# Kernel optimization log

Hardware: AMD Instinct MI355X
Metric: run time of the kernel (lower is better)

The kernel has to match this reference:

```python
import jax, jax.numpy as jnp
import numpy as np

N = 100000      # nodes
E = 1600000     # edges (avg degree 16)
F_IN = 64
HID = 128
OUT = 64


def setup_inputs() -> dict:
    key = jax.random.key(0)
    ks = jax.random.split(key, 12)
    s = lambda k, i, o: jax.random.normal(k, (i, o), jnp.float32) / np.sqrt(i)
    x = jax.random.normal(ks[0], (N, F_IN), jnp.float32)
    edge_index = jax.random.randint(ks[1], (2, E), 0, N, dtype=jnp.int64)
    return {
        "x": x,
        "edge_index": edge_index,
        # conv1: SAGEConv(F_IN -> HID): lin_l (neighbors, with bias), lin_r (root)
        "W1n": s(ks[2], F_IN, HID), "b1n": jnp.zeros((HID,), jnp.float32),
        "W1r": s(ks[3], F_IN, HID),
        # lin1: Linear(F_IN -> HID)
        "Wl1": s(ks[4], F_IN, HID), "bl1": jnp.zeros((HID,), jnp.float32),
        # conv2: SAGEConv(HID -> OUT)
        "W2n": s(ks[5], HID, OUT), "b2n": jnp.zeros((OUT,), jnp.float32),
        "W2r": s(ks[6], HID, OUT),
        # lin2: Linear(HID -> OUT)
        "Wl2": s(ks[7], HID, OUT), "bl2": jnp.zeros((OUT,), jnp.float32),
    }


def _sage(x, src, dst, Wn, bn, Wr):
    # mean aggregation of source-node features at destination nodes
    msg = x[src]                                             # [E, F]
    agg = jax.ops.segment_sum(msg, dst, num_segments=N)      # [N, F]
    deg = jax.ops.segment_sum(jnp.ones((src.shape[0],), x.dtype), dst,
                              num_segments=N)                # [N]
    mean = agg / jnp.maximum(deg, 1.0)[:, None]
    return mean @ Wn + bn + x @ Wr


def reference(x, edge_index, W1n, b1n, W1r, Wl1, bl1, W2n, b2n, W2r, Wl2, bl2):
    src, dst = edge_index[0], edge_index[1]
    h = _sage(x, src, dst, W1n, b1n, W1r) + (x @ Wl1 + bl1)
    h = jax.nn.relu(h)
    out = _sage(h, src, dst, W2n, b2n, W2r) + (h @ Wl2 + bl2)
    return out
```

## Files before the change

### kernel.cpp

```cpp
#include <hip/hip_runtime.h>


#define NN 100000
#define NE 1600000
#define NSB 98
#define CAP2 18432
#define EPB 6250

typedef __attribute__((ext_vector_type(8))) __bf16 bf16x8;
typedef __attribute__((ext_vector_type(4))) float f32x4;

__device__ __forceinline__ float b2f(unsigned short u) {
    unsigned v = ((unsigned)u) << 16;
    float f;
    __builtin_memcpy(&f, &v, 4);
    return f;
}
__device__ __forceinline__ float b2f_lo(unsigned v) {
    unsigned w = v << 16;
    float f;
    __builtin_memcpy(&f, &w, 4);
    return f;
}
__device__ __forceinline__ float b2f_hi(unsigned v) {
    unsigned w = v & 0xFFFF0000u;
    float f;
    __builtin_memcpy(&f, &w, 4);
    return f;
}
__device__ __forceinline__ unsigned short f2b(float f) {
    unsigned u;
    __builtin_memcpy(&u, &f, 4);
    u += 0x7FFFu + ((u >> 16) & 1u);
    return (unsigned short)(u >> 16);
}

__global__ void sniff_kernel(const int* __restrict__ ei,
                             const unsigned int* __restrict__ xw,
                             int* __restrict__ flags, int* __restrict__ cntP) {
    __shared__ int s_or[256];
    __shared__ int s_cnt[256];
    int tid = threadIdx.x;
    if (tid < NSB) cntP[tid * 16] = 0;
    s_or[tid] = ei[2 * tid + 1];
    unsigned e = (xw[tid] >> 7) & 0xFFu;
    s_cnt[tid] = (e > 0x85u) ? 1 : 0;
    __syncthreads();
    for (int s = 128; s > 0; s >>= 1) {
        if (tid < s) { s_or[tid] |= s_or[tid + s]; s_cnt[tid] += s_cnt[tid + s]; }
        __syncthreads();
    }
    if (tid == 0) {
        flags[0] = (s_or[0] == 0) ? 1 : 0;
        flags[1] = (s_cnt[0] >= 32) ? 1 : 0;
    }
}

__global__ __launch_bounds__(256) void prep_kernel(
    const void* __restrict__ x, const int* __restrict__ flags,
    const void* W1n, const void* W1r, const void* Wl1,
    const void* b1n, const void* bl1,
    const void* W2n, const void* W2r, const void* Wl2,
    const void* b2n, const void* bl2,
    unsigned short* __restrict__ Wt1g, unsigned short* __restrict__ Wt2g,
    float* __restrict__ bias1, float* __restrict__ bias2,
    unsigned int* __restrict__ xbu) {
    bool fp32 = flags[1] != 0;
    int tid = threadIdx.x;
    if (blockIdx.x >= 2) {
        int t = (blockIdx.x - 2) * 256 + tid;
        if (t >= NN * 8) return;
        if (fp32) {
            const float4* xf = (const float4*)x;
            float4 a = xf[2 * t], b = xf[2 * t + 1];
            uint4 o;
            o.x = f2b(a.x) | ((unsigned)f2b(a.y) << 16);
            o.y = f2b(a.z) | ((unsigned)f2b(a.w) << 16);
            o.z = f2b(b.x) | ((unsigned)f2b(b.y) << 16);
            o.w = f2b(b.z) | ((unsigned)f2b(b.w) << 16);
            ((uint4*)xbu)[t] = o;
        } else {
            ((uint4*)xbu)[t] = ((const uint4*)x)[t];
        }
        return;
    }
    auto rd = [&](const void* p, int i) -> float {
        return fp32 ? ((const float*)p)[i] : b2f(((const unsigned short*)p)[i]);
    };
    if (blockIdx.x == 0) {
        for (int idx = tid; idx < 128 * 128; idx += 256) {
            int k = idx >> 7, c = idx & 127;
            float v = (k < 64) ? rd(W1n, k * 128 + c)
                               : rd(W1r, (k - 64) * 128 + c) + rd(Wl1, (k - 64) * 128 + c);
            Wt1g[c * 128 + k] = f2b(v);
        }
        for (int c = tid; c < 128; c += 256) bias1[c] = rd(b1n, c) + rd(bl1, c);
    } else {
        for (int idx = tid; idx < 128 * 128; idx += 256) {
            int k = idx >> 7, c = idx & 127;
            float v = (c < 64) ? rd(W2n, k * 64 + c)
                               : rd(W2r, k * 64 + (c - 64)) + rd(Wl2, k * 64 + (c - 64));
            Wt2g[c * 128 + k] = f2b(v);
        }
        for (int c = tid; c < 64; c += 256) bias2[c] = rd(b2n, c) + rd(bl2, c);
    }
}


__global__ __launch_bounds__(512) void bscatter_kernel(
    const int* __restrict__ ei, const int* __restrict__ flags,
    int* __restrict__ cntP, int* __restrict__ ebuf) {
    __shared__ int lh[NSB];
    __shared__ int lbase[NSB];
    int t = threadIdx.x;
    if (t < NSB) lh[t] = 0;
    __syncthreads();
    int e0 = blockIdx.x * EPB;
    bool i64 = flags[0] != 0;
    for (int i = t; i < EPB; i += 512) {
        int e = e0 + i;
        int d = i64 ? (int)((const long long*)ei)[NE + e] : ei[NE + e];
        atomicAdd(&lh[d >> 10], 1);
    }
    __syncthreads();
    if (t < NSB) {
        int c = lh[t];
        lbase[t] = c ? atomicAdd(&cntP[t * 16], c) : 0;
        lh[t] = 0;
    }
    __syncthreads();
    for (int i = t; i < EPB; i += 512) {
        int e = e0 + i;
        int s, d;
        if (i64) { const long long* q = (const long long*)ei; s = (int)q[e]; d = (int)q[NE + e]; }
        else     { s = ei[e]; d = ei[NE + e]; }
        int sb = d >> 10;
        int r = lbase[sb] + atomicAdd(&lh[sb], 1);
        if (r < CAP2) ebuf[sb * CAP2 + r] = (s << 10) | (d & 1023);
    }
}

__global__ __launch_bounds__(512) void csr_build_kernel(
    const int* __restrict__ ebuf, const int* __restrict__ cntP,
    int* __restrict__ rpack, int* __restrict__ csr) {
    __shared__ int lcnt[1024];
    __shared__ int lsum[512];
    __shared__ int lcur[1024];
    int t = threadIdx.x, b = blockIdx.x;
    lcnt[t] = 0; lcnt[t + 512] = 0;
    __syncthreads();
    int base = b * CAP2;
    int cnt = min(cntP[b * 16], CAP2);
    for (int i = t; i < cnt; i += 512) atomicAdd(&lcnt[ebuf[base + i] & 1023], 1);
    __syncthreads();
    int c0 = lcnt[2 * t], c1 = lcnt[2 * t + 1];
    lsum[t] = c0 + c1;
    __syncthreads();
    for (int off = 1; off < 512; off <<= 1) {
        int v = lsum[t];
        int add = (t >= off) ? lsum[t - off] : 0;
        __syncthreads();
        lsum[t] = v + add;
        __syncthreads();
    }
    int excl = (t == 0) ? 0 : lsum[t - 1];
    int ex0 = excl, ex1 = excl + c0;
    lcur[2 * t] = ex0; lcur[2 * t + 1] = ex1;
    int d0 = b * 1024 + 2 * t;
    if (d0 < NN)     rpack[d0]     = ((base + ex0) << 8) | min(c0, 255);
    if (d0 + 1 < NN) rpack[d0 + 1] = ((base + ex1) << 8) | min(c1, 255);
    __syncthreads();
    for (int i = t; i < cnt; i += 512) {
        int pk = ebuf[base + i];
        int r = atomicAdd(&lcur[pk & 1023], 1);
        csr[base + r] = pk >> 10;
    }
}


__device__ __forceinline__ void gather_acc(
    const unsigned short* __restrict__ feat, const int* __restrict__ csr,
    int base, int deg, int fo, float* acc) {
    int t = 0;
    for (; t + 8 <= deg; t += 8) {
        int i0 = csr[base + t],     i1 = csr[base + t + 1];
        int i2 = csr[base + t + 2], i3 = csr[base + t + 3];
        int i4 = csr[base + t + 4], i5 = csr[base + t + 5];
        int i6 = csr[base + t + 6], i7 = csr[base + t + 7];
        bf16x8 v0 = *(const bf16x8*)(feat + (size_t)i0 * 64 + fo);
        bf16x8 v1 = *(const bf16x8*)(feat + (size_t)i1 * 64 + fo);
        bf16x8 v2 = *(const bf16x8*)(feat + (size_t)i2 * 64 + fo);
        bf16x8 v3 = *(const bf16x8*)(feat + (size_t)i3 * 64 + fo);
        bf16x8 v4 = *(const bf16x8*)(feat + (size_t)i4 * 64 + fo);
        bf16x8 v5 = *(const bf16x8*)(feat + (size_t)i5 * 64 + fo);
        bf16x8 v6 = *(const bf16x8*)(feat + (size_t)i6 * 64 + fo);
        bf16x8 v7 = *(const bf16x8*)(feat + (size_t)i7 * 64 + fo);
#pragma unroll
        for (int k = 0; k < 8; ++k)
            acc[k] += (((float)v0[k] + (float)v1[k]) + ((float)v2[k] + (float)v3[k]))
                    + (((float)v4[k] + (float)v5[k]) + ((float)v6[k] + (float)v7[k]));
    }
    for (; t + 4 <= deg; t += 4) {
        int i0 = csr[base + t],     i1 = csr[base + t + 1];
        int i2 = csr[base + t + 2], i3 = csr[base + t + 3];
        bf16x8 v0 = *(const bf16x8*)(feat + (size_t)i0 * 64 + fo);
        bf16x8 v1 = *(const bf16x8*)(feat + (size_t)i1 * 64 + fo);
        bf16x8 v2 = *(const bf16x8*)(feat + (size_t)i2 * 64 + fo);
        bf16x8 v3 = *(const bf16x8*)(feat + (size_t)i3 * 64 + fo);
#pragma unroll
        for (int k = 0; k < 8; ++k)
            acc[k] += ((float)v0[k] + (float)v1[k]) + ((float)v2[k] + (float)v3[k]);
    }
    for (; t < deg; ++t) {
        int i = csr[base + t];
        bf16x8 v = *(const bf16x8*)(feat + (size_t)i * 64 + fo);
#pragma unroll
        for (int k = 0; k < 8; ++k) acc[k] += (float)v[k];
    }
}

__global__ __launch_bounds__(256) void agg1_kernel(
    const unsigned short* __restrict__ feat, const int* __restrict__ rpack,
    const int* __restrict__ csr, unsigned int* __restrict__ mean1u) {
    int wid = threadIdx.x >> 6, lane = threadIdx.x & 63;
    int slot = lane >> 3, fo = (lane & 7) * 8;
    int d = (blockIdx.x * 4 + wid) * 8 + slot;
    int dd = min(d, NN - 1);
    int rp = rpack[dd];
    int base = rp >> 8;
    int deg = rp & 255;
    float acc[8];
#pragma unroll
    for (int k = 0; k < 8; ++k) acc[k] = 0.f;
    gather_acc(feat, csr, base, deg, fo, acc);
    if (d < NN) {
        float r = 1.0f / fmaxf((float)deg, 1.0f);
        uint4 o;
        o.x = f2b(acc[0] * r) | ((unsigned)f2b(acc[1] * r) << 16);
        o.y = f2b(acc[2] * r) | ((unsigned)f2b(acc[3] * r) << 16);
        o.z = f2b(acc[4] * r) | ((unsigned)f2b(acc[5] * r) << 16);
        o.w = f2b(acc[6] * r) | ((unsigned)f2b(acc[7] * r) << 16);
        *(uint4*)(mean1u + (size_t)d * 32 + (lane & 7) * 4) = o;
    }
}

__global__ __launch_bounds__(256) void agg2_kernel(
    const unsigned short* __restrict__ p, const int* __restrict__ rpack,
    const int* __restrict__ csr, const unsigned int* __restrict__ sfu,
    const float* __restrict__ bias2, const int* __restrict__ flags,
    void* __restrict__ out) {
    int wid = threadIdx.x >> 6, lane = threadIdx.x & 63;
    int slot = lane >> 3, fo = (lane & 7) * 8;
    int d = (blockIdx.x * 4 + wid) * 8 + slot;
    int dd = min(d, NN - 1);
    int rp = rpack[dd];
    int base = rp >> 8;
    int deg = rp & 255;
    float acc[8];
#pragma unroll
    for (int k = 0; k < 8; ++k) acc[k] = 0.f;
    gather_acc(p, csr, base, deg, fo, acc);
    if (d < NN) {
        float r = 1.0f / fmaxf((float)deg, 1.0f);
        uint4 sv = *(const uint4*)(sfu + (size_t)d * 32 + (lane & 7) * 4);
        float4 bA = *(const float4*)(bias2 + fo);
        float4 bB = *(const float4*)(bias2 + fo + 4);
        float v0 = acc[0] * r + b2f_lo(sv.x) + bA.x;
        float v1 = acc[1] * r + b2f_hi(sv.x) + bA.y;
        float v2 = acc[2] * r + b2f_lo(sv.y) + bA.z;
        float v3 = acc[3] * r + b2f_hi(sv.y) + bA.w;
        float v4 = acc[4] * r + b2f_lo(sv.z) + bB.x;
        float v5 = acc[5] * r + b2f_hi(sv.z) + bB.y;
        float v6 = acc[6] * r + b2f_lo(sv.w) + bB.z;
        float v7 = acc[7] * r + b2f_hi(sv.w) + bB.w;
        if (flags[1]) {
            float* op = (float*)out + (size_t)d * 64 + fo;
            *(float4*)op = make_float4(v0, v1, v2, v3);
            *(float4*)(op + 4) = make_float4(v4, v5, v6, v7);
        } else {
            uint4 o;
            o.x = f2b(v0) | ((unsigned)f2b(v1) << 16);
            o.y = f2b(v2) | ((unsigned)f2b(v3) << 16);
            o.z = f2b(v4) | ((unsigned)f2b(v5) << 16);
            o.w = f2b(v6) | ((unsigned)f2b(v7) << 16);
            *(uint4*)((unsigned int*)out + (size_t)d * 32 + (lane & 7) * 4) = o;
        }
    }
}

__global__ __launch_bounds__(256) void gemmF_kernel(
    const unsigned short* __restrict__ mean1,
    const unsigned short* __restrict__ xb,
    const unsigned short* __restrict__ Wt1g, const float* __restrict__ bias1,
    const unsigned short* __restrict__ Wt2g,
    unsigned short* __restrict__ p, unsigned short* __restrict__ sf) {
    __shared__ unsigned short Wt[128 * 136];
    __shared__ unsigned short hs[64 * 136];
    int tid = threadIdx.x;
    int wid = tid >> 6, lane = tid & 63;
    int m = lane & 15, g = lane >> 4;
    int row0 = blockIdx.x * 64 + wid * 16;
    int arow = min(row0 + m, NN - 1);

    bf16x8 a_frag[4];
#pragma unroll
    for (int kt = 0; kt < 4; ++kt) {
        int k0 = kt * 32 + g * 8;
        a_frag[kt] = (k0 < 64)
            ? *(const bf16x8*)(mean1 + (size_t)arow * 64 + k0)
            : *(const bf16x8*)(xb + (size_t)arow * 64 + (k0 - 64));
    }

    for (int idx = tid; idx < 2048; idx += 256) {
        int c = idx >> 4, ch = idx & 15;
        *(bf16x8*)&Wt[c * 136 + ch * 8] = *(const bf16x8*)&Wt1g[c * 128 + ch * 8];
    }
    __syncthreads();

    f32x4 acc[8];
#pragma unroll
    for (int nt = 0; nt < 8; ++nt) acc[nt] = (f32x4){0.f, 0.f, 0.f, 0.f};

#pragma unroll
    for (int kt = 0; kt < 4; ++kt) {
        int k0 = kt * 32 + g * 8;
#pragma unroll
        for (int nt = 0; nt < 8; ++nt) {
            bf16x8 b = *(const bf16x8*)(&Wt[(nt * 16 + m) * 136 + k0]);
            acc[nt] = __builtin_amdgcn_mfma_f32_16x16x32_bf16(a_frag[kt], b, acc[nt], 0, 0, 0);
        }
    }

#pragma unroll
    for (int nt = 0; nt < 8; ++nt) {
        int col = nt * 16 + m;
        float bias = bias1[col];
#pragma unroll
        for (int r = 0; r < 4; ++r) {
            float v = fmaxf(acc[nt][r] + bias, 0.0f);
            hs[(wid * 16 + g * 4 + r) * 136 + col] = f2b(v);
        }
    }

#pragma unroll
    for (int nt = 0; nt < 8; ++nt) acc[nt] = (f32x4){0.f, 0.f, 0.f, 0.f};

#pragma unroll
    for (int kt = 0; kt < 4; ++kt) {
        int k0 = kt * 32 + g * 8;
        bf16x8 a = *(const bf16x8*)(&hs[(wid * 16 + m) * 136 + k0]);
#pragma unroll
        for (int nt = 0; nt < 8; ++nt) {
            bf16x8 b = *(const bf16x8*)(&Wt2g[(nt * 16 + m) * 128 + k0]);
            acc[nt] = __builtin_amdgcn_mfma_f32_16x16x32_bf16(a, b, acc[nt], 0, 0, 0);
        }
    }

#pragma unroll
    for (int nt = 0; nt < 8; ++nt) {
        int col = nt * 16 + m;
#pragma unroll
        for (int r = 0; r < 4; ++r) {
            int row2 = row0 + g * 4 + r;
            if (row2 < NN) {
                float v = acc[nt][r];
                if (col < 64) p[(size_t)row2 * 64 + col] = f2b(v);
                else          sf[(size_t)row2 * 64 + (col - 64)] = f2b(v);
            }
        }
    }
}

extern "C" void kernel_launch(void* const* d_in, const int* in_sizes, int n_in,
                              void* d_out, int out_size, void* d_ws, size_t ws_size,
                              hipStream_t stream) {
    const void* x   = d_in[0];
    const int*  ei  = (const int*)d_in[1];
    const void* W1n = d_in[2];
    const void* b1n = d_in[3];
    const void* W1r = d_in[4];
    const void* Wl1 = d_in[5];
    const void* bl1 = d_in[6];
    const void* W2n = d_in[7];
    const void* b2n = d_in[8];
    const void* W2r = d_in[9];
    const void* Wl2 = d_in[10];
    const void* bl2 = d_in[11];

    char* ws = (char*)d_ws;
    int*            flags = (int*)(ws + 0);
    int*            cntP  = (int*)(ws + 1024);
    int*            rpack = (int*)(ws + 8192);
    float*          bias1 = (float*)(ws + 409600);
    float*          bias2 = (float*)(ws + 410112);
    unsigned short* Wt1g  = (unsigned short*)(ws + 410368);
    unsigned short* Wt2g  = (unsigned short*)(ws + 443136);
    int*            csr   = (int*)(ws + 475904);
    unsigned short* xb    = (unsigned short*)(ws + 7701248);
    unsigned short* p     = xb;
    unsigned short* mean1 = (unsigned short*)(ws + 20501248);
    unsigned short* sf    = (unsigned short*)(ws + 33301248);
    int*            ebuf  = (int*)(ws + 46101248);

    (void)in_sizes; (void)n_in; (void)out_size; (void)ws_size;

    sniff_kernel<<<1, 256, 0, stream>>>(ei, (const unsigned int*)x, flags, cntP);
    prep_kernel<<<2 + (NN * 8 + 255) / 256, 256, 0, stream>>>(
        x, flags, W1n, W1r, Wl1, b1n, bl1, W2n, W2r, Wl2, b2n, bl2,
        Wt1g, Wt2g, bias1, bias2, (unsigned int*)xb);
    bscatter_kernel<<<256, 512, 0, stream>>>(ei, flags, cntP, ebuf);
    csr_build_kernel<<<NSB, 512, 0, stream>>>(ebuf, cntP, rpack, csr);
    agg1_kernel<<<(NN + 31) / 32, 256, 0, stream>>>(xb, rpack, csr, (unsigned int*)mean1);
    gemmF_kernel<<<(NN + 63) / 64, 256, 0, stream>>>(mean1, xb, Wt1g, bias1, Wt2g, p, sf);
    agg2_kernel<<<(NN + 31) / 32, 256, 0, stream>>>(p, rpack, csr, (const unsigned int*)sf,
                                                    bias2, flags, d_out);
}
```

Baseline: 271.0 us.

## Enlarge fused GEMM tile to 256 rows and stage both weights in LDS

The fused two-layer GEMM kernel now processes 256 rows per block with 512 threads, and each wave computes two 16-row tiles that share the same B fragments. The second weight matrix is now loaded into shared memory alongside the first, replacing per-MFMA global reads. B fragments are preloaded into registers per k-step. This cuts redundant weight loads and global traffic in the second GEMM, at the cost of more LDS (about 138KB) and registers per block, fewer blocks, and lower occupancy.

```diff
diff --git a/kernel.cpp b/kernel.cpp
--- a/kernel.cpp
+++ b/kernel.cpp
@@ -6,6 +6,7 @@
 #define NSB 98
 #define CAP2 18432
 #define EPB 6250
+#define MB 256
 
 typedef __attribute__((ext_vector_type(8))) __bf16 bf16x8;
 typedef __attribute__((ext_vector_type(4))) float f32x4;
@@ -288,87 +289,116 @@
     }
 }
 
-__global__ __launch_bounds__(256) void gemmF_kernel(
+__global__ __launch_bounds__(512, 2) void gemmF_kernel(
     const unsigned short* __restrict__ mean1,
     const unsigned short* __restrict__ xb,
     const unsigned short* __restrict__ Wt1g, const float* __restrict__ bias1,
     const unsigned short* __restrict__ Wt2g,
     unsigned short* __restrict__ p, unsigned short* __restrict__ sf) {
-    __shared__ unsigned short Wt[128 * 136];
-    __shared__ unsigned short hs[64 * 136];
+    __shared__ unsigned short Wt1s[128 * 136];
+    __shared__ unsigned short Wt2s[128 * 136];
+    __shared__ unsigned short hs[MB * 136];
     int tid = threadIdx.x;
     int wid = tid >> 6, lane = tid & 63;
     int m = lane & 15, g = lane >> 4;
-    int row0 = blockIdx.x * 64 + wid * 16;
-    int arow = min(row0 + m, NN - 1);
-
-    bf16x8 a_frag[4];
+    int row0 = blockIdx.x * MB + wid * 32;
+
+    bf16x8 a_frag[2][4];
+#pragma unroll
+    for (int t = 0; t < 2; ++t) {
+        int arow = min(row0 + t * 16 + m, NN - 1);
+#pragma unroll
+        for (int kt = 0; kt < 4; ++kt) {
+            int k0 = kt * 32 + g * 8;
+            a_frag[t][kt] = (k0 < 64)
+                ? *(const bf16x8*)(mean1 + (size_t)arow * 64 + k0)
+                : *(const bf16x8*)(xb + (size_t)arow * 64 + (k0 - 64));
+        }
+    }
+
+    for (int idx = tid; idx < 4096; idx += 512) {
+        int c = (idx >> 4) & 127, ch = idx & 15;
+        if (idx < 2048)
+            *(bf16x8*)&Wt1s[c * 136 + ch * 8] = *(const bf16x8*)&Wt1g[c * 128 + ch * 8];
+        else
+            *(bf16x8*)&Wt2s[c * 136 + ch * 8] = *(const bf16x8*)&Wt2g[c * 128 + ch * 8];
+    }
+    __syncthreads();
+
+    f32x4 acc[2][8];
+#pragma unroll
+    for (int t = 0; t < 2; ++t)
+#pragma unroll
+        for (int nt = 0; nt < 8; ++nt) acc[t][nt] = (f32x4){0.f, 0.f, 0.f, 0.f};
+
 #pragma unroll
     for (int kt = 0; kt < 4; ++kt) {
         int k0 = kt * 32 + g * 8;
-        a_frag[kt] = (k0 < 64)
-            ? *(const bf16x8*)(mean1 + (size_t)arow * 64 + k0)
-            : *(const bf16x8*)(xb + (size_t)arow * 64 + (k0 - 64));
-    }
-
-    for (int idx = tid; idx < 2048; idx += 256) {
-        int c = idx >> 4, ch = idx & 15;
-        *(bf16x8*)&Wt[c * 136 + ch * 8] = *(const bf16x8*)&Wt1g[c * 128 + ch * 8];
-    }
-    __syncthreads();
-
-    f32x4 acc[8];
-#pragma unroll
-    for (int nt = 0; nt < 8; ++nt) acc[nt] = (f32x4){0.f, 0.f, 0.f, 0.f};
+        bf16x8 b[8];
+#pragma unroll
+        for (int nt = 0; nt < 8; ++nt)
+            b[nt] = *(const bf16x8*)(&Wt1s[(nt * 16 + m) * 136 + k0]);
+#pragma unroll
+        for (int nt = 0; nt < 8; ++nt) {
+            acc[0][nt] = __builtin_amdgcn_mfma_f32_16x16x32_bf16(a_frag[0][kt], b[nt], acc[0][nt], 0, 0, 0);
+            acc[1][nt] = __builtin_amdgcn_mfma_f32_16x16x32_bf16(a_frag[1][kt], b[nt], acc[1][nt], 0, 0, 0);
+        }
+    }
+
+#pragma unroll
+    for (int t = 0; t < 2; ++t)
+#pragma unroll
+        for (int nt = 0; nt < 8; ++nt) {
+            int col = nt * 16 + m;
+            float bias = bias1[col];
+#pragma unroll
+            for (int r = 0; r < 4; ++r) {
+                float v = fmaxf(acc[t][nt][r] + bias, 0.0f);
+                hs[(wid * 32 + t * 16 + g * 4 + r) * 136 + col] = f2b(v);
+            }
+        }
+
+    bf16x8 a2[2][4];
+#pragma unroll
+    for (int t = 0; t < 2; ++t)
+#pragma unroll
+        for (int kt = 0; kt < 4; ++kt)
+            a2[t][kt] = *(const bf16x8*)(&hs[(wid * 32 + t * 16 + m) * 136 + kt * 32 + g * 8]);
+
+#pragma unroll
+    for (int t = 0; t < 2; ++t)
+#pragma unroll
+        for (int nt = 0; nt < 8; ++nt) acc[t][nt] = (f32x4){0.f, 0.f, 0.f, 0.f};
 
 #pragma unroll
     for (int kt = 0; kt < 4; ++kt) {
         int k0 = kt * 32 + g * 8;
+        bf16x8 b[8];
+#pragma unroll
+        for (int nt = 0; nt < 8; ++nt)
+            b[nt] = *(const bf16x8*)(&Wt2s[(nt * 16 + m) * 136 + k0]);
 #pragma unroll
         for (int nt = 0; nt < 8; ++nt) {
-            bf16x8 b = *(const bf16x8*)(&Wt[(nt * 16 + m) * 136 + k0]);
-            acc[nt] = __builtin_amdgcn_mfma_f32_16x16x32_bf16(a_frag[kt], b, acc[nt], 0, 0, 0);
-        }
-    }
-
-#pragma unroll
-    for (int nt = 0; nt < 8; ++nt) {
-        int col = nt * 16 + m;
-        float bias = bias1[col];
-#pragma unroll
-        for (int r = 0; r < 4; ++r) {
-            float v = fmaxf(acc[nt][r] + bias, 0.0f);
-            hs[(wid * 16 + g * 4 + r) * 136 + col] = f2b(v);
-        }
-    }
-
-#pragma unroll
-    for (int nt = 0; nt < 8; ++nt) acc[nt] = (f32x4){0.f, 0.f, 0.f, 0.f};
-
-#pragma unroll
-    for (int kt = 0; kt < 4; ++kt) {
-        int k0 = kt * 32 + g * 8;
-        bf16x8 a = *(const bf16x8*)(&hs[(wid * 16 + m) * 136 + k0]);
+            acc[0][nt] = __builtin_amdgcn_mfma_f32_16x16x32_bf16(a2[0][kt], b[nt], acc[0][nt], 0, 0, 0);
+            acc[1][nt] = __builtin_amdgcn_mfma_f32_16x16x32_bf16(a2[1][kt], b[nt], acc[1][nt], 0, 0, 0);
+        }
+    }
+
+#pragma unroll
+    for (int t = 0; t < 2; ++t)
 #pragma unroll
         for (int nt = 0; nt < 8; ++nt) {
-            bf16x8 b = *(const bf16x8*)(&Wt2g[(nt * 16 + m) * 128 + k0]);
-            acc[nt] = __builtin_amdgcn_mfma_f32_16x16x32_bf16(a, b, acc[nt], 0, 0, 0);
-        }
-    }
-
-#pragma unroll
-    for (int nt = 0; nt < 8; ++nt) {
-        int col = nt * 16 + m;
-#pragma unroll
-        for (int r = 0; r < 4; ++r) {
-            int row2 = row0 + g * 4 + r;
-            if (row2 < NN) {
-                float v = acc[nt][r];
-                if (col < 64) p[(size_t)row2 * 64 + col] = f2b(v);
-                else          sf[(size_t)row2 * 64 + (col - 64)] = f2b(v);
+            int col = nt * 16 + m;
+#pragma unroll
+            for (int r = 0; r < 4; ++r) {
+                int row2 = row0 + t * 16 + g * 4 + r;
+                if (row2 < NN) {
+                    float v = acc[t][nt][r];
+                    if (col < 64) p[(size_t)row2 * 64 + col] = f2b(v);
+                    else          sf[(size_t)row2 * 64 + (col - 64)] = f2b(v);
+                }
             }
         }
-    }
 }
 
 extern "C" void kernel_launch(void* const* d_in, const int* in_sizes, int n_in,
@@ -411,7 +441,7 @@
     bscatter_kernel<<<256, 512, 0, stream>>>(ei, flags, cntP, ebuf);
     csr_build_kernel<<<NSB, 512, 0, stream>>>(ebuf, cntP, rpack, csr);
     agg1_kernel<<<(NN + 31) / 32, 256, 0, stream>>>(xb, rpack, csr, (unsigned int*)mean1);
-    gemmF_kernel<<<(NN + 63) / 64, 256, 0, stream>>>(mean1, xb, Wt1g, bias1, Wt2g, p, sf);
+    gemmF_kernel<<<(NN + MB - 1) / MB, 512, 0, stream>>>(mean1, xb, Wt1g, bias1, Wt2g, p, sf);
     agg2_kernel<<<(NN + 31) / 32, 256, 0, stream>>>(p, rpack, csr, (const unsigned int*)sf,
                                                     bias2, flags, d_out);
 }
```

After: 252.8 us. 1.07x faster.
